# Kernel optimization log

Hardware: AMD Instinct MI355X
Metric: run time of the kernel (lower is better)

Reference implementation:

```python
import jax, jax.numpy as jnp
import numpy as np
import math

REG = 0.1      # entropic regularization (self.reg)
TEMP = 0.1     # self.temperature from kwargs
ITERS = 20     # self.iters
EPS = 1e-5     # torch LayerNorm eps
ALPHA_BOTH = -100.0


def _layernorm(t, g, b):
    mu = jnp.mean(t, axis=-1, keepdims=True)
    var = jnp.mean((t - mu) ** 2, axis=-1, keepdims=True)
    return (t - mu) / jnp.sqrt(var + EPS) * g + b


def setup_inputs() -> dict:
    key = jax.random.key(0)
    k1, k2, k3 = jax.random.split(key, 3)
    B, M, N, H = 2048, 36, 36, 768
    x = jax.random.normal(k1, (B, M, H), jnp.float32)
    y = jax.random.normal(k2, (B, N, H), jnp.float32)
    # dustbin scorer params: LayerNorm(H) -> Linear(H, 1)
    ln_g = jnp.ones((H,), jnp.float32)
    ln_b = jnp.zeros((H,), jnp.float32)
    w = jax.random.normal(k3, (H, 1), jnp.float32) * (1.0 / math.sqrt(H))
    b_lin = jnp.zeros((1,), jnp.float32)
    return {"x": x, "y": y, "ln_g": ln_g, "ln_b": ln_b, "w": w, "b_lin": b_lin}


def reference(x, y, ln_g, ln_b, w, b_lin):
    B, M, H = x.shape
    N = y.shape[1]
    # CosineScorer(temperature=1).score(x, y, get_diag=False)
    xn = x / jnp.linalg.norm(x, axis=-1, keepdims=True)
    yn = y / jnp.linalg.norm(y, axis=-1, keepdims=True)
    scores = jnp.einsum('bmh,bnh->bmn', xn, yn)            # (B, M, N)
    # tanh-clipped learned dustbin scores
    ax = jnp.tanh(_layernorm(x, ln_g, ln_b) @ w + b_lin)   # (B, M, 1)
    ay = jnp.tanh(_layernorm(y, ln_g, ln_b) @ w + b_lin)   # (B, N, 1)
    # augmented score matrix with dustbin row/col
    alpha_both = jnp.full((B, 1, 1), ALPHA_BOTH, scores.dtype)
    top = jnp.concatenate([scores, ax], axis=2)                       # (B, M, N+1)
    bot = jnp.concatenate([jnp.swapaxes(ay, 1, 2), alpha_both], axis=2)  # (B, 1, N+1)
    couplings = jnp.concatenate([top, bot], axis=1) / REG             # (B, M+1, N+1)
    # SuperGlue-style marginals: dustbins absorb the complementary mass
    norm_c = -math.log(M + N)
    log_mu = jnp.concatenate([jnp.full((M,), norm_c),
                              jnp.array([math.log(N) + norm_c])]).astype(scores.dtype)
    log_nu = jnp.concatenate([jnp.full((N,), norm_c),
                              jnp.array([math.log(M) + norm_c])]).astype(scores.dtype)

    def body(carry, _):
        u, v = carry
        u = log_mu[None, :] - jax.nn.logsumexp(couplings + v[:, None, :], axis=2)
        v = log_nu[None, :] - jax.nn.logsumexp(couplings + u[:, :, None], axis=1)
        return (u, v), None

    u0 = jnp.zeros((B, M + 1), scores.dtype)
    v0 = jnp.zeros((B, N + 1), scores.dtype)
    (u, v), _ = jax.lax.scan(body, (u0, v0), None, length=ITERS)
    Z = couplings + u[:, :, None] + v[:, None, :] - norm_c            # log matching, (B, M+1, N+1)
    # scalar alignment score per batch element: <P, S> / temperature
    total = jnp.sum(jnp.exp(Z[:, :-1, :-1]) * scores, axis=(1, 2)) / TEMP
    return Z, total
```

## Files before the change

### kernel.cpp

```cpp
#include <hip/hip_runtime.h>
#include <stdint.h>
#include <stddef.h>


typedef float  f4  __attribute__((ext_vector_type(4)));
typedef short  s8v __attribute__((ext_vector_type(8)));
typedef unsigned int u2v __attribute__((ext_vector_type(2)));

#define HD   768
#define MR   36
#define KC   128
#define NCH  6
#define AS   136
#define CS   44
#define ITERS 20
#define LOG2E 1.4426950408889634f
#define LN2   0.6931471805599453f
#define L272  6.169925001442312f
#define KC2   (10.0f*LOG2E)
#define NEGB  (-1.0e30f)

__device__ __forceinline__ uint32_t pkbf2(float a, float b) {
    uint32_t ua = __float_as_uint(a), ub = __float_as_uint(b);
    ua += 0x7FFFu + ((ua >> 16) & 1u);
    ub += 0x7FFFu + ((ub >> 16) & 1u);
    return (ua >> 16) | (ub & 0xFFFF0000u);
}

__global__ __launch_bounds__(256, 4) void sinkhorn_kernel(
    const float* __restrict__ X, const float* __restrict__ Y,
    const float* __restrict__ LG, const float* __restrict__ LB,
    const float* __restrict__ W,  const float* __restrict__ BL,
    float* __restrict__ OUT, int NB)
{
    __shared__ __align__(16) uint16_t AB[72 * AS];
    __shared__ __align__(16) float C2 [37 * CS];
    __shared__ __align__(16) float u_l[40];
    __shared__ __align__(16) float v_l[40];
    __shared__ float stx[MR * 3], sty[MR * 3];
    __shared__ float rnx[MR], rny[MR];
    __shared__ float s_gw, s_bw, red[4];

    uint16_t* Al = AB;
    uint16_t* Bt = AB + 36 * AS;
    float*    C2T = (float*)AB;

    const int t  = threadIdx.x;
    const int b  = blockIdx.x;
    const int wv = t >> 6, ln = t & 63;
    const int c4 = t & 31, gg = t >> 5;

    if (t < 40) { u_l[t] = 0.0f; v_l[t] = 0.0f; }
    if (t < 37) {
        C2[t * CS + 37] = NEGB; C2[t * CS + 38] = NEGB; C2[t * CS + 39] = NEGB;
    }
    if (wv == 3) {
        float a = 0.0f, c = 0.0f;
        for (int q = 0; q < 12; ++q) {
            int h = ln + 64 * q;
            float wval = W[h];
            a += LG[h] * wval; c += LB[h] * wval;
        }
        for (int o = 32; o > 0; o >>= 1) { a += __shfl_down(a, o); c += __shfl_down(c, o); }
        if (ln == 0) { s_gw = a; s_bw = c; }
    }

    float sx[5][3], sy[5][3];
    #pragma unroll
    for (int p = 0; p < 5; ++p)
        #pragma unroll
        for (int s = 0; s < 3; ++s) { sx[p][s] = 0.0f; sy[p][s] = 0.0f; }

    f4 acc[3];
    #pragma unroll
    for (int i = 0; i < 3; ++i) acc[i] = (f4){0.0f, 0.0f, 0.0f, 0.0f};

    const float* xb = X + (size_t)b * (MR * HD);
    const float* yb = Y + (size_t)b * (MR * HD);

    const int frow = ln & 15, fq = ln >> 4;
    const int arR = wv * 16 + frow;
    const int rA  = ((arR < MR) ? arR : (MR - 1)) * AS + fq * 8;
    const int rB0 = (frow)      * AS + fq * 8;
    const int rB1 = (16 + frow) * AS + fq * 8;
    const int bt2 = 32 + frow;
    const int rB2 = ((bt2 < MR) ? bt2 : (MR - 1)) * AS + fq * 8;

    for (int kc = 0; kc < NCH; ++kc) {
        const int k0 = kc * KC;
        f4 gv = *(const f4*)(LG + k0 + c4 * 4);
        f4 wvec = *(const f4*)(W + k0 + c4 * 4);
        f4 gw = gv * wvec;
        #pragma unroll
        for (int p = 0; p < 5; ++p) {
            if (p < 4 || t < 128) {
                const int row = (p < 4) ? (p * 8 + gg) : (32 + gg);
                f4 xv = *(const f4*)(xb + row * HD + k0 + c4 * 4);
                sx[p][0] += (xv.x + xv.y) + (xv.z + xv.w);
                sx[p][1] += xv.x * xv.x + xv.y * xv.y + xv.z * xv.z + xv.w * xv.w;
                sx[p][2] += xv.x * gw.x + xv.y * gw.y + xv.z * gw.z + xv.w * gw.w;
                u2v px; px.x = pkbf2(xv.x, xv.y); px.y = pkbf2(xv.z, xv.w);
                *(u2v*)&Al[row * AS + c4 * 4] = px;
                f4 yv = *(const f4*)(yb + row * HD + k0 + c4 * 4);
                sy[p][0] += (yv.x + yv.y) + (yv.z + yv.w);
                sy[p][1] += yv.x * yv.x + yv.y * yv.y + yv.z * yv.z + yv.w * yv.w;
                sy[p][2] += yv.x * gw.x + yv.y * gw.y + yv.z * gw.z + yv.w * gw.w;
                u2v py; py.x = pkbf2(yv.x, yv.y); py.y = pkbf2(yv.z, yv.w);
                *(u2v*)&Bt[row * AS + c4 * 4] = py;
            }
        }
        __syncthreads();
        if (wv < 3) {
            #pragma unroll
            for (int ks = 0; ks < 4; ++ks) {
                s8v af = *(const s8v*)&Al[rA + ks * 32];
                s8v b0 = *(const s8v*)&Bt[rB0 + ks * 32];
                acc[0] = __builtin_amdgcn_mfma_f32_16x16x32_bf16(af, b0, acc[0], 0, 0, 0);
                s8v b1 = *(const s8v*)&Bt[rB1 + ks * 32];
                acc[1] = __builtin_amdgcn_mfma_f32_16x16x32_bf16(af, b1, acc[1], 0, 0, 0);
                s8v b2 = *(const s8v*)&Bt[rB2 + ks * 32];
                acc[2] = __builtin_amdgcn_mfma_f32_16x16x32_bf16(af, b2, acc[2], 0, 0, 0);
            }
        }
        __syncthreads();
    }

    #pragma unroll
    for (int p = 0; p < 5; ++p) {
        const int row = (p < 4) ? (p * 8 + gg) : (32 + gg);
        #pragma unroll
        for (int s = 0; s < 3; ++s) {
            float a = sx[p][s], c = sy[p][s];
            for (int o = 16; o > 0; o >>= 1) { a += __shfl_down(a, o, 32); c += __shfl_down(c, o, 32); }
            if ((t & 31) == 0 && row < MR) { stx[row * 3 + s] = a; sty[row * 3 + s] = c; }
        }
    }
    __syncthreads();

    {
        const float blin = BL[0];
        if (t < MR) {
            float Sx = stx[t * 3], Sxx = stx[t * 3 + 1], Sxw = stx[t * 3 + 2];
            rnx[t] = __builtin_amdgcn_rsqf(Sxx);
            float mu  = Sx * (1.0f / HD);
            float var = Sxx * (1.0f / HD) - mu * mu;
            float rsd = __builtin_amdgcn_rsqf(var + 1e-5f);
            float lin = (Sxw - mu * s_gw) * rsd + s_bw + blin;
            float e   = __builtin_amdgcn_exp2f(2.0f * LOG2E * lin);
            float th  = (e - 1.0f) / (e + 1.0f);
            C2 [t * CS + 36] = th * KC2;
            C2T[36 * CS + t] = th * KC2;
        } else if (t >= 64 && t < 64 + MR) {
            int j = t - 64;
            float Sy = sty[j * 3], Syy = sty[j * 3 + 1], Syw = sty[j * 3 + 2];
            rny[j] = __builtin_amdgcn_rsqf(Syy);
            float mu  = Sy * (1.0f / HD);
            float var = Syy * (1.0f / HD) - mu * mu;
            float rsd = __builtin_amdgcn_rsqf(var + 1e-5f);
            float lin = (Syw - mu * s_gw) * rsd + s_bw + blin;
            float e   = __builtin_amdgcn_exp2f(2.0f * LOG2E * lin);
            float th  = (e - 1.0f) / (e + 1.0f);
            C2 [36 * CS + j] = th * KC2;
            C2T[j * CS + 36] = th * KC2;
        } else if (t == 128) {
            C2 [36 * CS + 36] = -100.0f * KC2;
            C2T[36 * CS + 36] = -100.0f * KC2;
        } else if (t >= 192 && t < 192 + 37) {
            int r = t - 192;
            C2T[r * CS + 37] = NEGB; C2T[r * CS + 38] = NEGB; C2T[r * CS + 39] = NEGB;
        }
    }
    __syncthreads();

    if (wv < 3) {
        #pragma unroll
        for (int tn = 0; tn < 3; ++tn) {
            #pragma unroll
            for (int r = 0; r < 4; ++r) {
                int i = wv * 16 + fq * 4 + r;
                int j = tn * 16 + frow;
                if (i < MR && j < MR) {
                    float v = acc[tn][r] * rnx[i] * rny[j] * KC2;
                    C2 [i * CS + j] = v;
                    C2T[j * CS + i] = v;
                }
            }
        }
    }
    __syncthreads();

    const int sw = ((b >> 8) ^ b) & 3;
    if (wv == sw && ln < 37) {
        const int i = ln;
        const float lmu = (i < MR) ? -L272 : -1.0f;
        f4 cr[10], ct[10];
        #pragma unroll
        for (int jj = 0; jj < 10; ++jj) {
            cr[jj] = *(const f4*)(&C2 [i * CS + jj * 4]);
            ct[jj] = *(const f4*)(&C2T[i * CS + jj * 4]);
        }
        for (int it = 0; it < ITERS; ++it) {
            {
                f4 ea = (f4){0.0f,0.0f,0.0f,0.0f}, eb = (f4){0.0f,0.0f,0.0f,0.0f};
                #pragma unroll
                for (int jj = 0; jj < 10; ++jj) {
                    f4 sv = cr[jj] + *(const f4*)(&v_l[jj * 4]);
                    f4 ev;
                    ev.x = __builtin_amdgcn_exp2f(sv.x);
                    ev.y = __builtin_amdgcn_exp2f(sv.y);
                    ev.z = __builtin_amdgcn_exp2f(sv.z);
                    ev.w = __builtin_amdgcn_exp2f(sv.w);
                    if (jj & 1) eb += ev; else ea += ev;
                }
                f4 et = ea + eb;
                float ss = (et.x + et.y) + (et.z + et.w);
                u_l[i] = lmu - __builtin_amdgcn_logf(ss);
            }
            {
                f4 ea = (f4){0.0f,0.0f,0.0f,0.0f}, eb = (f4){0.0f,0.0f,0.0f,0.0f};
                #pragma unroll
                for (int jj = 0; jj < 10; ++jj) {
                    f4 sv = ct[jj] + *(const f4*)(&u_l[jj * 4]);
                    f4 ev;
                    ev.x = __builtin_amdgcn_exp2f(sv.x);
                    ev.y = __builtin_amdgcn_exp2f(sv.y);
                    ev.z = __builtin_amdgcn_exp2f(sv.z);
                    ev.w = __builtin_amdgcn_exp2f(sv.w);
                    if (jj & 1) eb += ev; else ea += ev;
                }
                f4 et = ea + eb;
                float ss = (et.x + et.y) + (et.z + et.w);
                v_l[i] = lmu - __builtin_amdgcn_logf(ss);
            }
        }
    }
    __syncthreads();

    float tot = 0.0f;
    const size_t ob = (size_t)b * 1369;
    for (int e = t; e < 1369; e += 256) {
        int i = e / 37, j = e - i * 37;
        float c2v = C2[i * CS + j];
        float z2  = c2v + u_l[i] + v_l[j] + L272;
        OUT[ob + e] = z2 * LN2;
        if (i < MR && j < MR)
            tot += __builtin_amdgcn_exp2f(z2) * (c2v * (0.1f * LN2));
    }
    for (int o = 32; o > 0; o >>= 1) tot += __shfl_down(tot, o);
    if (ln == 0) red[wv] = tot;
    __syncthreads();
    if (t == 0) OUT[(size_t)NB * 1369 + b] = (red[0] + red[1] + red[2] + red[3]) * 10.0f;
}

extern "C" void kernel_launch(void* const* d_in, const int* in_sizes, int n_in,
                              void* d_out, int out_size, void* d_ws, size_t ws_size,
                              hipStream_t stream) {
    const float* X  = (const float*)d_in[0];
    const float* Y  = (const float*)d_in[1];
    const float* LG = (const float*)d_in[2];
    const float* LB = (const float*)d_in[3];
    const float* W  = (const float*)d_in[4];
    const float* BL = (const float*)d_in[5];
    const int NB = in_sizes[0] / (MR * HD);
    hipLaunchKernelGGL(sinkhorn_kernel, dim3(NB), dim3(256), 0, stream,
                       X, Y, LG, LB, W, BL, (float*)d_out, NB);
}
```

Baseline: 505.6 us.

## Double-buffer LDS and register-prefetch input chunks to overlap loads with MFMA

Replaces the single-buffered chunk loop with a software pipeline. Two chunks of x/y are kept in registers so global loads for chunk k+2 are issued while chunk k is processed, and the shared tile is doubled so MFMA on one buffer overlaps with staging into the other. This also halves the barriers per chunk. It raises register and LDS use, so launch bounds drop to 3 blocks per CU, which may reduce occupancy and latency hiding across blocks.

New measurement: 666.1 us. +31.7%, slower.

```diff
diff --git a/kernel.cpp b/kernel.cpp
--- a/kernel.cpp
+++ b/kernel.cpp
@@ -27,13 +27,69 @@
     return (ua >> 16) | (ub & 0xFFFF0000u);
 }
 
-__global__ __launch_bounds__(256, 4) void sinkhorn_kernel(
+#define LOADCHUNK(KCI, XS, YS) {                                          \
+    const int k0_ = (KCI) * KC;                                           \
+    _Pragma("unroll")                                                     \
+    for (int p = 0; p < 5; ++p) {                                         \
+        if (p < 4 || t < 128) {                                           \
+            const int row_ = (p < 4) ? (p * 8 + gg) : (32 + gg);          \
+            XS[p] = *(const f4*)(xp + row_ * HD + k0_ + c4 * 4);          \
+            YS[p] = *(const f4*)(yp + row_ * HD + k0_ + c4 * 4);          \
+        }                                                                 \
+    }                                                                     \
+}
+
+#define PROCCHUNK(KCI, XS, YS) {                                          \
+    const int k0_ = (KCI) * KC;                                           \
+    f4 gvv = *(const f4*)(LG + k0_ + c4 * 4);                             \
+    f4 wvv = *(const f4*)(W  + k0_ + c4 * 4);                             \
+    f4 gw  = gvv * wvv;                                                   \
+    uint16_t* Alc = AB + ((KCI) & 1) * (72 * AS);                         \
+    uint16_t* Btc = Alc + 36 * AS;                                        \
+    _Pragma("unroll")                                                     \
+    for (int p = 0; p < 5; ++p) {                                         \
+        if (p < 4 || t < 128) {                                           \
+            const int row_ = (p < 4) ? (p * 8 + gg) : (32 + gg);          \
+            f4 xv = XS[p];                                                \
+            sx[p][0] += (xv.x + xv.y) + (xv.z + xv.w);                    \
+            sx[p][1] += xv.x*xv.x + xv.y*xv.y + xv.z*xv.z + xv.w*xv.w;    \
+            sx[p][2] += xv.x*gw.x + xv.y*gw.y + xv.z*gw.z + xv.w*gw.w;    \
+            u2v px; px.x = pkbf2(xv.x, xv.y); px.y = pkbf2(xv.z, xv.w);   \
+            *(u2v*)&Alc[row_ * AS + c4 * 4] = px;                         \
+            f4 yv = YS[p];                                                \
+            sy[p][0] += (yv.x + yv.y) + (yv.z + yv.w);                    \
+            sy[p][1] += yv.x*yv.x + yv.y*yv.y + yv.z*yv.z + yv.w*yv.w;    \
+            sy[p][2] += yv.x*gw.x + yv.y*gw.y + yv.z*gw.z + yv.w*gw.w;    \
+            u2v py; py.x = pkbf2(yv.x, yv.y); py.y = pkbf2(yv.z, yv.w);   \
+            *(u2v*)&Btc[row_ * AS + c4 * 4] = py;                         \
+        }                                                                 \
+    }                                                                     \
+}
+
+#define MFMACHUNK(KCI) {                                                  \
+    if (wv < 3) {                                                         \
+        const uint16_t* Alc = AB + ((KCI) & 1) * (72 * AS);               \
+        const uint16_t* Btc = Alc + 36 * AS;                              \
+        _Pragma("unroll")                                                 \
+        for (int ks = 0; ks < 4; ++ks) {                                  \
+            s8v af = *(const s8v*)&Alc[rA + ks * 32];                     \
+            s8v b0 = *(const s8v*)&Btc[rB0 + ks * 32];                    \
+            acc[0] = __builtin_amdgcn_mfma_f32_16x16x32_bf16(af, b0, acc[0], 0, 0, 0); \
+            s8v b1 = *(const s8v*)&Btc[rB1 + ks * 32];                    \
+            acc[1] = __builtin_amdgcn_mfma_f32_16x16x32_bf16(af, b1, acc[1], 0, 0, 0); \
+            s8v b2 = *(const s8v*)&Btc[rB2 + ks * 32];                    \
+            acc[2] = __builtin_amdgcn_mfma_f32_16x16x32_bf16(af, b2, acc[2], 0, 0, 0); \
+        }                                                                 \
+    }                                                                     \
+}
+
+__global__ __launch_bounds__(256, 3) void sinkhorn_kernel(
     const float* __restrict__ X, const float* __restrict__ Y,
     const float* __restrict__ LG, const float* __restrict__ LB,
     const float* __restrict__ W,  const float* __restrict__ BL,
     float* __restrict__ OUT, int NB)
 {
-    __shared__ __align__(16) uint16_t AB[72 * AS];
+    __shared__ __align__(16) uint16_t AB[144 * AS];
     __shared__ __align__(16) float C2 [37 * CS];
     __shared__ __align__(16) float u_l[40];
     __shared__ __align__(16) float v_l[40];
@@ -41,9 +97,7 @@
     __shared__ float rnx[MR], rny[MR];
     __shared__ float s_gw, s_bw, red[4];
 
-    uint16_t* Al = AB;
-    uint16_t* Bt = AB + 36 * AS;
-    float*    C2T = (float*)AB;
+    float* C2T = (float*)AB;
 
     const int t  = threadIdx.x;
     const int b  = blockIdx.x;
@@ -75,8 +129,8 @@
     #pragma unroll
     for (int i = 0; i < 3; ++i) acc[i] = (f4){0.0f, 0.0f, 0.0f, 0.0f};
 
-    const float* xb = X + (size_t)b * (MR * HD);
-    const float* yb = Y + (size_t)b * (MR * HD);
+    const float* xp = X + (size_t)b * (MR * HD);
+    const float* yp = Y + (size_t)b * (MR * HD);
 
     const int frow = ln & 15, fq = ln >> 4;
     const int arR = wv * 16 + frow;
@@ -86,43 +140,19 @@
     const int bt2 = 32 + frow;
     const int rB2 = ((bt2 < MR) ? bt2 : (MR - 1)) * AS + fq * 8;
 
-    for (int kc = 0; kc < NCH; ++kc) {
-        const int k0 = kc * KC;
-        f4 gv = *(const f4*)(LG + k0 + c4 * 4);
-        f4 wvec = *(const f4*)(W + k0 + c4 * 4);
-        f4 gw = gv * wvec;
-        #pragma unroll
-        for (int p = 0; p < 5; ++p) {
-            if (p < 4 || t < 128) {
-                const int row = (p < 4) ? (p * 8 + gg) : (32 + gg);
-                f4 xv = *(const f4*)(xb + row * HD + k0 + c4 * 4);
-                sx[p][0] += (xv.x + xv.y) + (xv.z + xv.w);
-                sx[p][1] += xv.x * xv.x + xv.y * xv.y + xv.z * xv.z + xv.w * xv.w;
-                sx[p][2] += xv.x * gw.x + xv.y * gw.y + xv.z * gw.z + xv.w * gw.w;
-                u2v px; px.x = pkbf2(xv.x, xv.y); px.y = pkbf2(xv.z, xv.w);
-                *(u2v*)&Al[row * AS + c4 * 4] = px;
-                f4 yv = *(const f4*)(yb + row * HD + k0 + c4 * 4);
-                sy[p][0] += (yv.x + yv.y) + (yv.z + yv.w);
-                sy[p][1] += yv.x * yv.x + yv.y * yv.y + yv.z * yv.z + yv.w * yv.w;
-                sy[p][2] += yv.x * gw.x + yv.y * gw.y + yv.z * gw.z + yv.w * gw.w;
-                u2v py; py.x = pkbf2(yv.x, yv.y); py.y = pkbf2(yv.z, yv.w);
-                *(u2v*)&Bt[row * AS + c4 * 4] = py;
-            }
-        }
+    f4 xA[5], yA[5], xB[5], yB[5];
+    LOADCHUNK(0, xA, yA);
+    LOADCHUNK(1, xB, yB);
+    #pragma unroll
+    for (int kk = 0; kk < 3; ++kk) {
+        PROCCHUNK(2 * kk, xA, yA);
+        if (2 * kk + 2 < NCH) LOADCHUNK(2 * kk + 2, xA, yA);
         __syncthreads();
-        if (wv < 3) {
-            #pragma unroll
-            for (int ks = 0; ks < 4; ++ks) {
-                s8v af = *(const s8v*)&Al[rA + ks * 32];
-                s8v b0 = *(const s8v*)&Bt[rB0 + ks * 32];
-                acc[0] = __builtin_amdgcn_mfma_f32_16x16x32_bf16(af, b0, acc[0], 0, 0, 0);
-                s8v b1 = *(const s8v*)&Bt[rB1 + ks * 32];
-                acc[1] = __builtin_amdgcn_mfma_f32_16x16x32_bf16(af, b1, acc[1], 0, 0, 0);
-                s8v b2 = *(const s8v*)&Bt[rB2 + ks * 32];
-                acc[2] = __builtin_amdgcn_mfma_f32_16x16x32_bf16(af, b2, acc[2], 0, 0, 0);
-            }
-        }
+        MFMACHUNK(2 * kk);
+        PROCCHUNK(2 * kk + 1, xB, yB);
+        if (2 * kk + 3 < NCH) LOADCHUNK(2 * kk + 3, xB, yB);
         __syncthreads();
+        MFMACHUNK(2 * kk + 1);
     }
 
     #pragma unroll
```

## Split fused kernel into score and single-wave Sinkhorn kernels via global staging

Applied to the files above, without the earlier changes.

Splits the single fused kernel in two. The first, a 256-thread kernel, computes the scaled cosine scores and dustbin entries and writes the coupling matrix to the output buffer. The second, a 64-thread kernel, reloads that matrix, runs the Sinkhorn iterations and writes the final log-matching and totals. This is meant to stop three idle waves from occupying a 256-thread block during the serial Sinkhorn loop, and to hoist all global loads in the score kernel ahead of the math. The cost is an extra global round trip of the coupling matrix and a second kernel launch.

Result: faster. 495.0 us (-2.1%).

```diff
diff --git a/kernel.cpp b/kernel.cpp
--- a/kernel.cpp
+++ b/kernel.cpp
@@ -27,7 +27,20 @@
     return (ua >> 16) | (ub & 0xFFFF0000u);
 }
 
-__global__ __launch_bounds__(256, 4) void sinkhorn_kernel(
+#define STEP(P, XV, YV, ROW) {                                             \
+    sx[P][0] += (XV.x + XV.y) + (XV.z + XV.w);                             \
+    sx[P][1] += XV.x*XV.x + XV.y*XV.y + XV.z*XV.z + XV.w*XV.w;             \
+    sx[P][2] += XV.x*gw.x + XV.y*gw.y + XV.z*gw.z + XV.w*gw.w;             \
+    u2v px; px.x = pkbf2(XV.x, XV.y); px.y = pkbf2(XV.z, XV.w);            \
+    *(u2v*)&Al[(ROW) * AS + c4 * 4] = px;                                  \
+    sy[P][0] += (YV.x + YV.y) + (YV.z + YV.w);                             \
+    sy[P][1] += YV.x*YV.x + YV.y*YV.y + YV.z*YV.z + YV.w*YV.w;             \
+    sy[P][2] += YV.x*gw.x + YV.y*gw.y + YV.z*gw.z + YV.w*gw.w;             \
+    u2v py; py.x = pkbf2(YV.x, YV.y); py.y = pkbf2(YV.z, YV.w);            \
+    *(u2v*)&Bt[(ROW) * AS + c4 * 4] = py;                                  \
+}
+
+__global__ __launch_bounds__(256, 4) void score_kernel(
     const float* __restrict__ X, const float* __restrict__ Y,
     const float* __restrict__ LG, const float* __restrict__ LB,
     const float* __restrict__ W,  const float* __restrict__ BL,
@@ -35,25 +48,18 @@
 {
     __shared__ __align__(16) uint16_t AB[72 * AS];
     __shared__ __align__(16) float C2 [37 * CS];
-    __shared__ __align__(16) float u_l[40];
-    __shared__ __align__(16) float v_l[40];
     __shared__ float stx[MR * 3], sty[MR * 3];
     __shared__ float rnx[MR], rny[MR];
-    __shared__ float s_gw, s_bw, red[4];
+    __shared__ float s_gw, s_bw;
 
     uint16_t* Al = AB;
     uint16_t* Bt = AB + 36 * AS;
-    float*    C2T = (float*)AB;
 
     const int t  = threadIdx.x;
     const int b  = blockIdx.x;
     const int wv = t >> 6, ln = t & 63;
     const int c4 = t & 31, gg = t >> 5;
 
-    if (t < 40) { u_l[t] = 0.0f; v_l[t] = 0.0f; }
-    if (t < 37) {
-        C2[t * CS + 37] = NEGB; C2[t * CS + 38] = NEGB; C2[t * CS + 39] = NEGB;
-    }
     if (wv == 3) {
         float a = 0.0f, c = 0.0f;
         for (int q = 0; q < 12; ++q) {
@@ -77,6 +83,9 @@
 
     const float* xb = X + (size_t)b * (MR * HD);
     const float* yb = Y + (size_t)b * (MR * HD);
+
+    const int r0 = gg, r1 = 8 + gg, r2 = 16 + gg, r3 = 24 + gg;
+    const int r4 = (t < 128) ? (32 + gg) : 35;
 
     const int frow = ln & 15, fq = ln >> 4;
     const int arR = wv * 16 + frow;
@@ -88,27 +97,27 @@
 
     for (int kc = 0; kc < NCH; ++kc) {
         const int k0 = kc * KC;
-        f4 gv = *(const f4*)(LG + k0 + c4 * 4);
-        f4 wvec = *(const f4*)(W + k0 + c4 * 4);
+        const float* xr = xb + k0 + c4 * 4;
+        const float* yr = yb + k0 + c4 * 4;
+        f4 gv   = *(const f4*)(LG + k0 + c4 * 4);
+        f4 wvec = *(const f4*)(W  + k0 + c4 * 4);
+        f4 x0 = *(const f4*)(xr + r0 * HD);
+        f4 y0 = *(const f4*)(yr + r0 * HD);
+        f4 x1 = *(const f4*)(xr + r1 * HD);
+        f4 y1 = *(const f4*)(yr + r1 * HD);
+        f4 x2 = *(const f4*)(xr + r2 * HD);
+        f4 y2 = *(const f4*)(yr + r2 * HD);
+        f4 x3 = *(const f4*)(xr + r3 * HD);
+        f4 y3 = *(const f4*)(yr + r3 * HD);
+        f4 x4 = *(const f4*)(xr + r4 * HD);
+        f4 y4 = *(const f4*)(yr + r4 * HD);
+        __builtin_amdgcn_sched_group_barrier(0x20, 12, 0);
         f4 gw = gv * wvec;
-        #pragma unroll
-        for (int p = 0; p < 5; ++p) {
-            if (p < 4 || t < 128) {
-                const int row = (p < 4) ? (p * 8 + gg) : (32 + gg);
-                f4 xv = *(const f4*)(xb + row * HD + k0 + c4 * 4);
-                sx[p][0] += (xv.x + xv.y) + (xv.z + xv.w);
-                sx[p][1] += xv.x * xv.x + xv.y * xv.y + xv.z * xv.z + xv.w * xv.w;
-                sx[p][2] += xv.x * gw.x + xv.y * gw.y + xv.z * gw.z + xv.w * gw.w;
-                u2v px; px.x = pkbf2(xv.x, xv.y); px.y = pkbf2(xv.z, xv.w);
-                *(u2v*)&Al[row * AS + c4 * 4] = px;
-                f4 yv = *(const f4*)(yb + row * HD + k0 + c4 * 4);
-                sy[p][0] += (yv.x + yv.y) + (yv.z + yv.w);
-                sy[p][1] += yv.x * yv.x + yv.y * yv.y + yv.z * yv.z + yv.w * yv.w;
-                sy[p][2] += yv.x * gw.x + yv.y * gw.y + yv.z * gw.z + yv.w * gw.w;
-                u2v py; py.x = pkbf2(yv.x, yv.y); py.y = pkbf2(yv.z, yv.w);
-                *(u2v*)&Bt[row * AS + c4 * 4] = py;
-            }
-        }
+        STEP(0, x0, y0, r0);
+        STEP(1, x1, y1, r1);
+        STEP(2, x2, y2, r2);
+        STEP(3, x3, y3, r3);
+        STEP(4, x4, y4, r4);
         __syncthreads();
         if (wv < 3) {
             #pragma unroll
@@ -148,8 +157,7 @@
             float lin = (Sxw - mu * s_gw) * rsd + s_bw + blin;
             float e   = __builtin_amdgcn_exp2f(2.0f * LOG2E * lin);
             float th  = (e - 1.0f) / (e + 1.0f);
-            C2 [t * CS + 36] = th * KC2;
-            C2T[36 * CS + t] = th * KC2;
+            C2[t * CS + 36] = th * KC2;
         } else if (t >= 64 && t < 64 + MR) {
             int j = t - 64;
             float Sy = sty[j * 3], Syy = sty[j * 3 + 1], Syw = sty[j * 3 + 2];
@@ -160,14 +168,9 @@
             float lin = (Syw - mu * s_gw) * rsd + s_bw + blin;
             float e   = __builtin_amdgcn_exp2f(2.0f * LOG2E * lin);
             float th  = (e - 1.0f) / (e + 1.0f);
-            C2 [36 * CS + j] = th * KC2;
-            C2T[j * CS + 36] = th * KC2;
+            C2[36 * CS + j] = th * KC2;
         } else if (t == 128) {
-            C2 [36 * CS + 36] = -100.0f * KC2;
-            C2T[36 * CS + 36] = -100.0f * KC2;
-        } else if (t >= 192 && t < 192 + 37) {
-            int r = t - 192;
-            C2T[r * CS + 37] = NEGB; C2T[r * CS + 38] = NEGB; C2T[r * CS + 39] = NEGB;
+            C2[36 * CS + 36] = -100.0f * KC2;
         }
     }
     __syncthreads();
@@ -179,18 +182,46 @@
             for (int r = 0; r < 4; ++r) {
                 int i = wv * 16 + fq * 4 + r;
                 int j = tn * 16 + frow;
-                if (i < MR && j < MR) {
-                    float v = acc[tn][r] * rnx[i] * rny[j] * KC2;
-                    C2 [i * CS + j] = v;
-                    C2T[j * CS + i] = v;
-                }
-            }
-        }
-    }
-    __syncthreads();
-
-    const int sw = ((b >> 8) ^ b) & 3;
-    if (wv == sw && ln < 37) {
+                if (i < MR && j < MR)
+                    C2[i * CS + j] = acc[tn][r] * rnx[i] * rny[j] * KC2;
+            }
+        }
+    }
+    __syncthreads();
+
+    const size_t ob = (size_t)b * 1369;
+    for (int e = t; e < 1369; e += 256) {
+        int i = e / 37, j = e - i * 37;
+        OUT[ob + e] = C2[i * CS + j];
+    }
+}
+
+__global__ __launch_bounds__(64, 2) void sinkhorn_kernel(
+    float* __restrict__ OUT, int NB)
+{
+    __shared__ __align__(16) float C2 [37 * CS];
+    __shared__ __align__(16) float C2T[37 * CS];
+    __shared__ __align__(16) float u_l[40];
+    __shared__ __align__(16) float v_l[40];
+
+    const int ln = threadIdx.x;
+    const int b  = blockIdx.x;
+    const size_t ob = (size_t)b * 1369;
+
+    if (ln < 40) { u_l[ln] = 0.0f; v_l[ln] = 0.0f; }
+    if (ln < 37) {
+        C2 [ln * CS + 37] = NEGB; C2 [ln * CS + 38] = NEGB; C2 [ln * CS + 39] = NEGB;
+        C2T[ln * CS + 37] = NEGB; C2T[ln * CS + 38] = NEGB; C2T[ln * CS + 39] = NEGB;
+    }
+    for (int e = ln; e < 1369; e += 64) {
+        int i = e / 37, j = e - i * 37;
+        float c = OUT[ob + e];
+        C2 [i * CS + j] = c;
+        C2T[j * CS + i] = c;
+    }
+    __syncthreads();
+
+    if (ln < 37) {
         const int i = ln;
         const float lmu = (i < MR) ? -L272 : -1.0f;
         f4 cr[10], ct[10];
@@ -237,8 +268,7 @@
     __syncthreads();
 
     float tot = 0.0f;
-    const size_t ob = (size_t)b * 1369;
-    for (int e = t; e < 1369; e += 256) {
+    for (int e = ln; e < 1369; e += 64) {
         int i = e / 37, j = e - i * 37;
         float c2v = C2[i * CS + j];
         float z2  = c2v + u_l[i] + v_l[j] + L272;
@@ -247,9 +277,7 @@
             tot += __builtin_amdgcn_exp2f(z2) * (c2v * (0.1f * LN2));
     }
     for (int o = 32; o > 0; o >>= 1) tot += __shfl_down(tot, o);
-    if (ln == 0) red[wv] = tot;
-    __syncthreads();
-    if (t == 0) OUT[(size_t)NB * 1369 + b] = (red[0] + red[1] + red[2] + red[3]) * 10.0f;
+    if (ln == 0) OUT[(size_t)NB * 1369 + b] = tot * 10.0f;
 }
 
 extern "C" void kernel_launch(void* const* d_in, const int* in_sizes, int n_in,
@@ -262,6 +290,8 @@
     const float* W  = (const float*)d_in[4];
     const float* BL = (const float*)d_in[5];
     const int NB = in_sizes[0] / (MR * HD);
-    hipLaunchKernelGGL(sinkhorn_kernel, dim3(NB), dim3(256), 0, stream,
+    hipLaunchKernelGGL(score_kernel, dim3(NB), dim3(256), 0, stream,
                        X, Y, LG, LB, W, BL, (float*)d_out, NB);
-}
+    hipLaunchKernelGGL(sinkhorn_kernel, dim3(NB), dim3(64), 0, stream,
+                       (float*)d_out, NB);
+}
```
